# Kernel tuning notes

Measured on AMD Instinct MI355X. Metric: run time of the kernel, lower is better.

## Reference

```python
import jax, jax.numpy as jnp
import numpy as np

N, K, D, C, H = 200000, 256, 12, 9, 32
EPS = 1e-8


def setup_inputs() -> dict:
    key = jax.random.key(0)
    ks = jax.random.split(key, 8)
    probe_pos = jax.random.uniform(ks[0], (N, 3), dtype=jnp.float32)
    mu = jax.random.uniform(ks[1], (K, 3), dtype=jnp.float32)
    log_s = jax.random.normal(ks[2], (K, 3), dtype=jnp.float32) * 0.3 - 1.5
    # quaternions near identity (w~1) as in the torch init
    q = jax.random.normal(ks[3], (K, 4), dtype=jnp.float32) * 0.1 + jnp.array([1.0, 0.0, 0.0, 0.0], jnp.float32)
    F = jax.random.normal(ks[4], (K, D), dtype=jnp.float32) * 0.1
    W1 = jax.random.normal(ks[5], (D + 3, H), dtype=jnp.float32) / np.sqrt(D + 3).astype(np.float32)
    b1 = jnp.zeros((H,), jnp.float32)
    W2 = jax.random.normal(ks[6], (H, C), dtype=jnp.float32) / np.sqrt(H).astype(np.float32)
    b2 = jnp.zeros((C,), jnp.float32)
    return {"probe_pos": probe_pos, "mu": mu, "log_s": log_s, "q": q,
            "F": F, "W1": W1, "b1": b1, "W2": W2, "b2": b2}


def quaternion_to_rotation_matrix(q):
    # q: [K,4] (w,x,y,z) -> [K,3,3]
    q = q / (jnp.linalg.norm(q, axis=-1, keepdims=True) + EPS)
    w, x, y, z = q[..., 0], q[..., 1], q[..., 2], q[..., 3]
    r0 = jnp.stack([1 - 2 * y * y - 2 * z * z, 2 * x * y - 2 * w * z, 2 * x * z + 2 * w * y], axis=-1)
    r1 = jnp.stack([2 * x * y + 2 * w * z, 1 - 2 * x * x - 2 * z * z, 2 * y * z - 2 * w * x], axis=-1)
    r2 = jnp.stack([2 * x * z - 2 * w * y, 2 * y * z + 2 * w * x, 1 - 2 * x * x - 2 * y * y], axis=-1)
    return jnp.stack([r0, r1, r2], axis=-2)


def reference(probe_pos, mu, log_s, q, F, W1, b1, W2, b2):
    s = jnp.exp(log_s)                                   # [K,3]
    R = quaternion_to_rotation_matrix(q)                 # [K,3,3]
    s_inv_sq = 1.0 / (s ** 2 + EPS)                      # [K,3]
    # precision = R @ diag(s_inv_sq) @ R^T -> [K,3,3]
    precision = jnp.einsum('kij,kj,klj->kil', R, s_inv_sq, R)
    diff = probe_pos[:, None, :] - mu[None, :, :]        # [N,K,3]
    mahal = jnp.einsum('nki,kij,nkj->nk', diff, precision, diff)  # [N,K]
    gvals = jnp.exp(-0.5 * mahal)                        # [N,K]
    radii = 3.0 * s.max(axis=1)                          # [K]
    dist = jnp.linalg.norm(diff, axis=2)                 # [N,K]
    gvals = gvals * (dist < radii[None, :]).astype(gvals.dtype)
    weights = gvals / (gvals.sum(axis=1, keepdims=True) + EPS)    # [N,K]
    latent = weights @ F                                 # [N,D]
    mlp_in = jnp.concatenate([latent, probe_pos], axis=1)         # [N,D+3]
    h = jax.nn.relu(mlp_in @ W1 + b1)                    # [N,H]
    sh = h @ W2 + b2                                     # [N,C]
    return (sh, latent, weights)
```

## Files before the change

kernel.cpp:

```cpp
#include <hip/hip_runtime.h>

#define KG 256
#define DD 12
#define HH 32
#define CC 9
#define TPB 256
#define PPB 64
#define KSPL 4
#define KPT 64
#define PSTR 16

typedef float f32x2 __attribute__((ext_vector_type(2)));

__global__ __launch_bounds__(256) void gp_pre(
    const float* __restrict__ mu, const float* __restrict__ log_s,
    const float* __restrict__ q, const float* __restrict__ F,
    float* __restrict__ Ct) {
  int k = threadIdx.x;
  if (k >= KG) return;
  float qw = q[k*4+0], qx = q[k*4+1], qy = q[k*4+2], qz = q[k*4+3];
  float nrm = sqrtf(qw*qw + qx*qx + qy*qy + qz*qz);
  float isn = 1.0f / (nrm + 1e-8f);
  qw *= isn; qx *= isn; qy *= isn; qz *= isn;
  float R00 = 1.f - 2.f*(qy*qy + qz*qz);
  float R01 = 2.f*(qx*qy - qw*qz);
  float R02 = 2.f*(qx*qz + qw*qy);
  float R10 = 2.f*(qx*qy + qw*qz);
  float R11 = 1.f - 2.f*(qx*qx + qz*qz);
  float R12 = 2.f*(qy*qz - qw*qx);
  float R20 = 2.f*(qx*qz - qw*qy);
  float R21 = 2.f*(qy*qz + qw*qx);
  float R22 = 1.f - 2.f*(qx*qx + qy*qy);
  float s0 = expf(log_s[k*3+0]);
  float s1 = expf(log_s[k*3+1]);
  float s2 = expf(log_s[k*3+2]);
  float si0 = 1.f/(s0*s0 + 1e-8f);
  float si1 = 1.f/(s1*s1 + 1e-8f);
  float si2 = 1.f/(s2*s2 + 1e-8f);
  float P00 = R00*si0*R00 + R01*si1*R01 + R02*si2*R02;
  float P01 = R00*si0*R10 + R01*si1*R11 + R02*si2*R12;
  float P02 = R00*si0*R20 + R01*si1*R21 + R02*si2*R22;
  float P11 = R10*si0*R10 + R11*si1*R11 + R12*si2*R12;
  float P12 = R10*si0*R20 + R11*si1*R21 + R12*si2*R22;
  float P22 = R20*si0*R20 + R21*si1*R21 + R22*si2*R22;
  float m0 = mu[k*3+0], m1 = mu[k*3+1], m2 = mu[k*3+2];
  float b0 = P00*m0 + P01*m1 + P02*m2;
  float b1v = P01*m0 + P11*m1 + P12*m2;
  float b2v = P02*m0 + P12*m1 + P22*m2;
  float cterm = m0*b0 + m1*b1v + m2*b2v;
  const float f = -0.7213475204444817f;
  float* c = Ct + k*32;
  c[0] = f*P00;  c[1] = f*P11;  c[2] = f*P22;
  c[3] = 2.f*f*P01;  c[4] = 2.f*f*P02;  c[5] = 2.f*f*P12;
  c[6] = -2.f*f*b0;  c[7] = -2.f*f*b1v; c[8] = -2.f*f*b2v;
  c[9] = f*cterm;
  c[10] = -2.f*m0;  c[11] = -2.f*m1;  c[12] = -2.f*m2;
  c[13] = m0*m0 + m1*m1 + m2*m2;
  float smax = fmaxf(s0, fmaxf(s1, s2));
  c[14] = (3.f*smax)*(3.f*smax);
  c[15] = 0.f;
  #pragma unroll
  for (int d = 0; d < DD; ++d) c[16+d] = F[k*DD + d];
  c[28] = c[29] = c[30] = c[31] = 0.f;
}

__device__ __forceinline__ float gauss_eval(
    const float* __restrict__ c,
    float xx, float yy, float zz, float xy, float xz, float yz,
    float x, float y, float z, float pp) {
  float tp = fmaf(c[0], xx, c[9]);
  tp = fmaf(c[1], yy, tp);
  tp = fmaf(c[2], zz, tp);
  tp = fmaf(c[3], xy, tp);
  tp = fmaf(c[4], xz, tp);
  tp = fmaf(c[5], yz, tp);
  tp = fmaf(c[6], x, tp);
  tp = fmaf(c[7], y, tp);
  tp = fmaf(c[8], z, tp);
  float d2 = pp + c[13];
  d2 = fmaf(c[10], x, d2);
  d2 = fmaf(c[11], y, d2);
  d2 = fmaf(c[12], z, d2);
  float e = __builtin_amdgcn_exp2f(tp);
  return (d2 < c[14]) ? e : 0.0f;
}

__global__ __launch_bounds__(TPB, 5) void gp_main(
    const float* __restrict__ pos, const float* __restrict__ Ct,
    const float* __restrict__ W1, const float* __restrict__ b1,
    const float* __restrict__ W2, const float* __restrict__ b2,
    float* __restrict__ sh_out, float* __restrict__ lat_out,
    float* __restrict__ w_out, int N) {
  __shared__ float part[KSPL * PPB * PSTR];
  __shared__ float4 pxyzi[PPB];
  const int tid  = threadIdx.x;
  const int lane = tid & 63;
  const int wv   = tid >> 6;
  const int pbase = blockIdx.x * PPB;

  if (tid < PPB) {
    int p = pbase + tid; if (p >= N) p = N - 1;
    pxyzi[tid] = make_float4(pos[p*3+0], pos[p*3+1], pos[p*3+2], 0.f);
  }
  __syncthreads();

  const float4 pv = pxyzi[lane];
  const float x = pv.x, y = pv.y, z = pv.z;
  const float xx = x*x, yy = y*y, zz = z*z;
  const float xy = x*y, xz = x*z, yz = y*z;
  const float pp = xx + yy + zz;

  const int kg = __builtin_amdgcn_readfirstlane(wv);
  const float* cbase = Ct + (size_t)(kg * KPT) * 32;
  f32x2 lat2[6];
  #pragma unroll
  for (int j = 0; j < 6; ++j) lat2[j] = (f32x2){0.f, 0.f};
  float dsum = 0.0f;
  #pragma unroll 4
  for (int i = 0; i < KPT; ++i) {
    const float* c = cbase + (i << 5);
    float g = gauss_eval(c, xx, yy, zz, xy, xz, yz, x, y, z, pp);
    dsum += g;
    const f32x2 g2 = (f32x2){g, g};
    const f32x2* f2 = (const f32x2*)(c + 16);
    #pragma unroll
    for (int j = 0; j < 6; ++j)
      lat2[j] = __builtin_elementwise_fma(g2, f2[j], lat2[j]);
  }
  {
    float* pw = part + (wv * PPB + lane) * PSTR;
    *(float4*)(pw + 0) = make_float4(lat2[0].x, lat2[0].y, lat2[1].x, lat2[1].y);
    *(float4*)(pw + 4) = make_float4(lat2[2].x, lat2[2].y, lat2[3].x, lat2[3].y);
    *(float4*)(pw + 8) = make_float4(lat2[4].x, lat2[4].y, lat2[5].x, lat2[5].y);
    *(float4*)(pw +12) = make_float4(dsum, 0.f, 0.f, 0.f);
  }
  __syncthreads();

  float cb[4][16];
  #pragma unroll
  for (int u = 0; u < 4; ++u) {
    const float4* r = (const float4*)(Ct + (((lane << 2) + u) << 5));
    *(float4*)&cb[u][0]  = r[0];
    *(float4*)&cb[u][4]  = r[1];
    *(float4*)&cb[u][8]  = r[2];
    *(float4*)&cb[u][12] = r[3];
  }

  #pragma unroll
  for (int s = tid; s < PPB*13; s += TPB) {
    const int pr = s / 13, j = s - pr*13;
    float a = part[(0*PPB + pr)*PSTR + j] + part[(1*PPB + pr)*PSTR + j]
            + part[(2*PPB + pr)*PSTR + j] + part[(3*PPB + pr)*PSTR + j];
    if (j == 12) pxyzi[pr].w = 1.0f / (a + 1e-8f);
    else part[pr*PSTR + j] = a;
  }
  __syncthreads();

  if (tid < PPB*3) {
    const int pr = tid / 3, q = tid - pr*3;
    if (pbase + pr < N) {
      const float iv = pxyzi[pr].w;
      const float* r = part + pr*PSTR + q*4;
      *(float4*)(lat_out + (size_t)pbase*DD + tid*4) =
          make_float4(r[0]*iv, r[1]*iv, r[2]*iv, r[3]*iv);
    }
  }

  if (tid < PPB && pbase + tid < N) {
    const float inv = pxyzi[tid].w;
    float in15[15];
    #pragma unroll
    for (int j = 0; j < DD; ++j) in15[j] = part[tid*PSTR + j] * inv;
    in15[12] = x; in15[13] = y; in15[14] = z;
    float o[CC];
    #pragma unroll
    for (int c2 = 0; c2 < CC; ++c2) o[c2] = b2[c2];
    #pragma unroll 2
    for (int j = 0; j < HH; ++j) {
      float a = b1[j];
      #pragma unroll
      for (int i = 0; i < 15; ++i) a = fmaf(in15[i], W1[i*HH + j], a);
      a = fmaxf(a, 0.f);
      #pragma unroll
      for (int c2 = 0; c2 < CC; ++c2) o[c2] = fmaf(a, W2[j*CC + c2], o[c2]);
    }
    float* so = sh_out + (size_t)(pbase + tid) * CC;
    #pragma unroll
    for (int c2 = 0; c2 < CC; ++c2) so[c2] = o[c2];
  }

  #pragma unroll 2
  for (int pi = 0; pi < PPB/KSPL; ++pi) {
    const int lp = (wv << 4) + pi;
    const float4 b = pxyzi[lp];
    const float bx = b.x, by = b.y, bz = b.z, binv = b.w;
    const float bxx = bx*bx, byy = by*by, bzz = bz*bz;
    const float bxy = bx*by, bxz = bx*bz, byz = by*bz;
    const float bpp = bxx + byy + bzz;
    float wq[4];
    #pragma unroll
    for (int u = 0; u < 4; ++u)
      wq[u] = gauss_eval(cb[u], bxx, byy, bzz, bxy, bxz, byz,
                         bx, by, bz, bpp) * binv;
    const int gp2 = pbase + lp;
    if (gp2 < N)
      *(float4*)&w_out[(size_t)gp2 * KG + (lane << 2)] =
          make_float4(wq[0], wq[1], wq[2], wq[3]);
  }
}

extern "C" void kernel_launch(void* const* d_in, const int* in_sizes, int n_in,
                              void* d_out, int out_size, void* d_ws, size_t ws_size,
                              hipStream_t stream) {
  const float* probe_pos = (const float*)d_in[0];
  const float* mu        = (const float*)d_in[1];
  const float* log_s     = (const float*)d_in[2];
  const float* q         = (const float*)d_in[3];
  const float* F         = (const float*)d_in[4];
  const float* W1        = (const float*)d_in[5];
  const float* b1        = (const float*)d_in[6];
  const float* W2        = (const float*)d_in[7];
  const float* b2        = (const float*)d_in[8];
  const int N = in_sizes[0] / 3;

  float* Ct = (float*)d_ws;
  float* sh_out  = (float*)d_out;
  float* lat_out = sh_out + (size_t)N*CC;
  float* w_out   = lat_out + (size_t)N*DD;

  gp_pre<<<1, 256, 0, stream>>>(mu, log_s, q, F, Ct);
  const int nb = (N + PPB - 1) / PPB;
  gp_main<<<nb, TPB, 0, stream>>>(probe_pos, Ct, W1, b1, W2, b2,
                                  sh_out, lat_out, w_out, N);
}
```

Measured before the change: 289.9 us.

## Process two probes per thread to reuse Gaussian coefficients across points

```diff
diff --git a/kernel.cpp b/kernel.cpp
--- a/kernel.cpp
+++ b/kernel.cpp
@@ -5,10 +5,10 @@
 #define HH 32
 #define CC 9
 #define TPB 256
-#define PPB 64
+#define PPB 128
 #define KSPL 4
 #define KPT 64
-#define PSTR 16
+#define PSTR 14
 
 typedef float f32x2 __attribute__((ext_vector_type(2)));
 
@@ -104,35 +104,50 @@
   }
   __syncthreads();
 
-  const float4 pv = pxyzi[lane];
-  const float x = pv.x, y = pv.y, z = pv.z;
-  const float xx = x*x, yy = y*y, zz = z*z;
-  const float xy = x*y, xz = x*z, yz = y*z;
-  const float pp = xx + yy + zz;
+  const float4 pva = pxyzi[lane];
+  const float4 pvb = pxyzi[lane + 64];
+  const float xa = pva.x, ya = pva.y, za = pva.z;
+  const float xb = pvb.x, yb = pvb.y, zb = pvb.z;
+  const float xxa = xa*xa, yya = ya*ya, zza = za*za;
+  const float xya = xa*ya, xza = xa*za, yza = ya*za;
+  const float ppa = xxa + yya + zza;
+  const float xxb = xb*xb, yyb = yb*yb, zzb = zb*zb;
+  const float xyb = xb*yb, xzb = xb*zb, yzb = yb*zb;
+  const float ppb = xxb + yyb + zzb;
 
   const int kg = __builtin_amdgcn_readfirstlane(wv);
   const float* cbase = Ct + (size_t)(kg * KPT) * 32;
-  f32x2 lat2[6];
-  #pragma unroll
-  for (int j = 0; j < 6; ++j) lat2[j] = (f32x2){0.f, 0.f};
-  float dsum = 0.0f;
-  #pragma unroll 4
+  f32x2 lat2a[6], lat2b[6];
+  #pragma unroll
+  for (int j = 0; j < 6; ++j) { lat2a[j] = (f32x2){0.f,0.f}; lat2b[j] = (f32x2){0.f,0.f}; }
+  float dsuma = 0.0f, dsumb = 0.0f;
+  #pragma unroll 2
   for (int i = 0; i < KPT; ++i) {
     const float* c = cbase + (i << 5);
-    float g = gauss_eval(c, xx, yy, zz, xy, xz, yz, x, y, z, pp);
-    dsum += g;
-    const f32x2 g2 = (f32x2){g, g};
+    float ga = gauss_eval(c, xxa, yya, zza, xya, xza, yza, xa, ya, za, ppa);
+    float gb = gauss_eval(c, xxb, yyb, zzb, xyb, xzb, yzb, xb, yb, zb, ppb);
+    dsuma += ga;
+    dsumb += gb;
+    const f32x2 g2a = (f32x2){ga, ga};
+    const f32x2 g2b = (f32x2){gb, gb};
     const f32x2* f2 = (const f32x2*)(c + 16);
     #pragma unroll
-    for (int j = 0; j < 6; ++j)
-      lat2[j] = __builtin_elementwise_fma(g2, f2[j], lat2[j]);
+    for (int j = 0; j < 6; ++j) {
+      lat2a[j] = __builtin_elementwise_fma(g2a, f2[j], lat2a[j]);
+      lat2b[j] = __builtin_elementwise_fma(g2b, f2[j], lat2b[j]);
+    }
   }
   {
     float* pw = part + (wv * PPB + lane) * PSTR;
-    *(float4*)(pw + 0) = make_float4(lat2[0].x, lat2[0].y, lat2[1].x, lat2[1].y);
-    *(float4*)(pw + 4) = make_float4(lat2[2].x, lat2[2].y, lat2[3].x, lat2[3].y);
-    *(float4*)(pw + 8) = make_float4(lat2[4].x, lat2[4].y, lat2[5].x, lat2[5].y);
-    *(float4*)(pw +12) = make_float4(dsum, 0.f, 0.f, 0.f);
+    *(f32x2*)(pw + 0) = lat2a[0]; *(f32x2*)(pw + 2) = lat2a[1];
+    *(f32x2*)(pw + 4) = lat2a[2]; *(f32x2*)(pw + 6) = lat2a[3];
+    *(f32x2*)(pw + 8) = lat2a[4]; *(f32x2*)(pw +10) = lat2a[5];
+    pw[12] = dsuma;
+    float* qw2 = part + (wv * PPB + lane + 64) * PSTR;
+    *(f32x2*)(qw2 + 0) = lat2b[0]; *(f32x2*)(qw2 + 2) = lat2b[1];
+    *(f32x2*)(qw2 + 4) = lat2b[2]; *(f32x2*)(qw2 + 6) = lat2b[3];
+    *(f32x2*)(qw2 + 8) = lat2b[4]; *(f32x2*)(qw2 +10) = lat2b[5];
+    qw2[12] = dsumb;
   }
   __syncthreads();
 
@@ -156,22 +171,24 @@
   }
   __syncthreads();
 
-  if (tid < PPB*3) {
-    const int pr = tid / 3, q = tid - pr*3;
+  #pragma unroll
+  for (int s = tid; s < PPB*3; s += TPB) {
+    const int pr = s / 3, q = s - pr*3;
     if (pbase + pr < N) {
       const float iv = pxyzi[pr].w;
       const float* r = part + pr*PSTR + q*4;
-      *(float4*)(lat_out + (size_t)pbase*DD + tid*4) =
+      *(float4*)(lat_out + (size_t)pbase*DD + s*4) =
           make_float4(r[0]*iv, r[1]*iv, r[2]*iv, r[3]*iv);
     }
   }
 
   if (tid < PPB && pbase + tid < N) {
-    const float inv = pxyzi[tid].w;
+    const float4 pm = pxyzi[tid];
+    const float inv = pm.w;
     float in15[15];
     #pragma unroll
     for (int j = 0; j < DD; ++j) in15[j] = part[tid*PSTR + j] * inv;
-    in15[12] = x; in15[13] = y; in15[14] = z;
+    in15[12] = pm.x; in15[13] = pm.y; in15[14] = pm.z;
     float o[CC];
     #pragma unroll
     for (int c2 = 0; c2 < CC; ++c2) o[c2] = b2[c2];
@@ -191,7 +208,7 @@
 
   #pragma unroll 2
   for (int pi = 0; pi < PPB/KSPL; ++pi) {
-    const int lp = (wv << 4) + pi;
+    const int lp = (wv << 5) + pi;
     const float4 b = pxyzi[lp];
     const float bx = b.x, by = b.y, bz = b.z, binv = b.w;
     const float bxx = bx*bx, byy = by*by, bzz = bz*bz;
```

Result: no change. 291.1 us (+0.4%).
